# Performance work log

Hardware: AMD Instinct MI355X
Metric: run time of the kernel (lower is better)

Reference implementation:

```python
import jax, jax.numpy as jnp
import numpy as np

PATCH = 16  # patch_size

def _patchify(images, p=PATCH):
    # images: [B, H, W] -> patches: [B, N, p*p] in raster order
    B, H, W = images.shape
    x = images.reshape(B, H // p, p, W // p, p)
    x = x.transpose(0, 1, 3, 2, 4)  # [B, H/p, W/p, p, p]
    return x.reshape(B, (H // p) * (W // p), p * p)

def setup_inputs() -> dict:
    key = jax.random.key(0)
    k1, k2 = jax.random.split(key)
    images = jax.random.normal(k1, (64, 256, 256), dtype=jnp.float32)
    vocab = jax.random.normal(k2, (4096, 256), dtype=jnp.float32)  # [V, patch^2]
    return {"images": images, "vocab": vocab}

def reference(images, vocab):
    # forward_patches: patchify (raster ordering -> identity permutation)
    patches = _patchify(images)  # [B, N, D]
    # forward_tokens: torch.cdist + argmin. argmin of Euclidean distance
    # equals argmin of squared distance; expand ||x-v||^2 to avoid the
    # explicit [B, N, V, D] difference tensor.
    v2 = jnp.sum(vocab * vocab, axis=-1)                      # [V]
    xv = jnp.einsum('bnd,vd->bnv', patches, vocab)            # [B, N, V]
    x2 = jnp.sum(patches * patches, axis=-1, keepdims=True)   # [B, N, 1]
    d2 = x2 - 2.0 * xv + v2                                   # [B, N, V]
    tokens = jnp.argmin(d2, axis=-1)                          # [B, N] int
    return patches, tokens
```

## Files before the change

kernel.cpp:

```cpp
#include <hip/hip_runtime.h>
#include <math.h>

#define PS      16
#define D       256
#define V       4096
#define M       16384
#define NSPLIT  32
#define PAIR_CAP 1048576
#define QMARGIN 130

typedef _Float16 half8 __attribute__((ext_vector_type(8)));
typedef _Float16 half4 __attribute__((ext_vector_type(4)));
typedef float    f32x4 __attribute__((ext_vector_type(4)));

__device__ __forceinline__ void gload_lds16(const void* g, void* l) {
  __builtin_amdgcn_global_load_lds(
      (const __attribute__((address_space(1))) unsigned int*)g,
      (__attribute__((address_space(3))) unsigned int*)l, 16, 0, 0);
}

__global__ __launch_bounds__(256) void patchify_half_kernel(
    const float* __restrict__ img, float* __restrict__ outp,
    _Float16* __restrict__ Ah, int* __restrict__ paircount) {
  if (blockIdx.x == 0 && threadIdx.x == 0) *paircount = 0;
  const int t  = blockIdx.x * 256 + threadIdx.x;
  const int o4 = t << 2;
  const int b   = o4 >> 16;
  const int rem = o4 & 65535;
  const int n   = rem >> 8;
  const int d   = rem & 255;
  const int py = n >> 4, px = n & 15, i = d >> 4, j = d & 15;
  const float4 v = *(const float4*)(img + (b << 16) + ((py * PS + i) << 8) + px * PS + j);
  *(float4*)(outp + o4) = v;
  half4 h = { (_Float16)v.x, (_Float16)v.y, (_Float16)v.z, (_Float16)v.w };
  *(half4*)(Ah + o4) = h;
}

__global__ __launch_bounds__(256) void vocab_half_v2_kernel(
    const float* __restrict__ vocab, _Float16* __restrict__ Vh,
    float* __restrict__ v2) {
  const int gtid = blockIdx.x * 256 + threadIdx.x;
  const int row  = gtid >> 6;
  const int lane = gtid & 63;
  const float4 v = *(const float4*)(vocab + (size_t)row * D + (lane << 2));
  half4 h = { (_Float16)v.x, (_Float16)v.y, (_Float16)v.z, (_Float16)v.w };
  *(half4*)(Vh + (size_t)row * D + (lane << 2)) = h;
  float s = v.x * v.x + v.y * v.y + v.z * v.z + v.w * v.w;
  #pragma unroll
  for (int off = 32; off > 0; off >>= 1) s += __shfl_down(s, off);
  if (lane == 0) v2[row] = s;
}

__global__ __launch_bounds__(256, 3) void gemm_score_kernel(
    const _Float16* __restrict__ Ah,
    const _Float16* __restrict__ Vh,
    const float* __restrict__ v2,
    unsigned* __restrict__ pk1, unsigned* __restrict__ pk2) {
  __shared__ __align__(16) _Float16 Af[8 * 64 * 32];
  __shared__ unsigned eK1[64][4];
  __shared__ unsigned eK2[64][4];

  const int tid  = threadIdx.x;
  const int lane = tid & 63;
  const int wid  = tid >> 6;
  const int cb   = blockIdx.x;
  const int row0 = blockIdx.y * 64;
  const int col0 = cb * 128 + wid * 32;

  {
    const int srow = lane >> 2;
    const int sg   = ((lane & 3) ^ ((srow >> 1) & 3)) << 3;
    const _Float16* Ag = Ah + (size_t)(row0 + wid * 16 + srow) * D + sg;
    _Float16* Al = Af + wid * 16 * 32;
    #pragma unroll
    for (int kt = 0; kt < 8; ++kt)
      gload_lds16(Ag + kt * 32, Al + kt * 64 * 32);
  }
  __syncthreads();

  const int cl = lane & 15;
  const int q  = lane >> 4;
  const int fg = (q ^ ((cl >> 1) & 3)) << 3;
  const _Float16* Ab = Af + cl * 32 + fg;

  const int c0 = col0 + cl;
  const int c1 = c0 + 16;
  const _Float16* B0 = Vh + (size_t)c0 * D + q * 8;
  const _Float16* B1 = Vh + (size_t)c1 * D + q * 8;

  f32x4 acc[4][2];
  #pragma unroll
  for (int i = 0; i < 4; ++i) {
    acc[i][0] = (f32x4){0.f, 0.f, 0.f, 0.f};
    acc[i][1] = (f32x4){0.f, 0.f, 0.f, 0.f};
  }

  #pragma unroll 1
  for (int kt = 0; kt < 8; ++kt) {
    const half8 b0 = *(const half8*)(B0 + kt * 32);
    const half8 b1 = *(const half8*)(B1 + kt * 32);
    half8 af[4];
    #pragma unroll
    for (int i = 0; i < 4; ++i)
      af[i] = *(const half8*)(Ab + kt * 2048 + i * 512);
    #pragma unroll
    for (int i = 0; i < 4; ++i) {
      acc[i][0] = __builtin_amdgcn_mfma_f32_16x16x32_f16(af[i], b0, acc[i][0], 0, 0, 0);
      acc[i][1] = __builtin_amdgcn_mfma_f32_16x16x32_f16(af[i], b1, acc[i][1], 0, 0, 0);
    }
  }

  const float C0 = fmaf(v2[c0], 512.0f, 524288.0f);
  const float C1 = fmaf(v2[c1], 512.0f, 524288.0f);
  unsigned kk1[16], kk2[16];
  #pragma unroll
  for (int i = 0; i < 4; ++i)
    #pragma unroll
    for (int r = 0; r < 4; ++r) {
      const int p = i * 4 + r;
      const unsigned k0 = ((unsigned)fmaf(-1024.0f, acc[i][0][r], C0) << 12) | (unsigned)c0;
      const unsigned k1 = ((unsigned)fmaf(-1024.0f, acc[i][1][r], C1) << 12) | (unsigned)c1;
      kk1[p] = min(k0, k1);
      kk2[p] = max(k0, k1);
    }
  #pragma unroll
  for (int p = 0; p < 16; ++p) {
    unsigned k1 = kk1[p], k2 = kk2[p];
    #pragma unroll
    for (int mask = 1; mask <= 8; mask <<= 1) {
      const unsigned o1 = (unsigned)__shfl_xor((int)k1, mask);
      const unsigned o2 = (unsigned)__shfl_xor((int)k2, mask);
      k2 = min(min(k2, o2), max(k1, o1));
      k1 = min(k1, o1);
    }
    kk1[p] = k1; kk2[p] = k2;
  }
  if (cl == 0) {
    #pragma unroll
    for (int p = 0; p < 16; ++p) {
      const int rl = (p >> 2) * 16 + q * 4 + (p & 3);
      eK1[rl][wid] = kk1[p]; eK2[rl][wid] = kk2[p];
    }
  }
  __syncthreads();
  if (tid < 64) {
    unsigned K1 = 0xFFFFFFFFu, K2 = 0xFFFFFFFFu;
    #pragma unroll
    for (int w = 0; w < 4; ++w) {
      const unsigned b1 = eK1[tid][w], b2 = eK2[tid][w];
      K2 = min(min(K2, b2), max(K1, b1));
      K1 = min(K1, b1);
    }
    pk1[(size_t)cb * M + row0 + tid] = K1;
    pk2[(size_t)cb * M + row0 + tid] = K2;
  }
}

__global__ __launch_bounds__(256) void reduce_gather_kernel(
    const unsigned* __restrict__ pk1, const unsigned* __restrict__ pk2,
    float* __restrict__ tok, unsigned long long* __restrict__ minkey,
    unsigned* __restrict__ pairs, int* __restrict__ paircount) {
  const int m = blockIdx.x * 256 + threadIdx.x;
  unsigned K1 = 0xFFFFFFFFu, K2 = 0xFFFFFFFFu;
  for (int s = 0; s < NSPLIT; ++s) {
    const unsigned b1 = pk1[(size_t)s * M + m];
    const unsigned b2 = pk2[(size_t)s * M + m];
    K2 = min(min(K2, b2), max(K1, b1));
    K1 = min(K1, b1);
  }
  tok[m] = (float)(K1 & 4095u);
  minkey[m] = 0xFFFFFFFFFFFFFFFFull;
  if ((int)(K2 >> 12) - (int)(K1 >> 12) <= QMARGIN) {
    const int th = (int)(K1 >> 12) + QMARGIN;
    int cnt = 0;
    for (int s = 0; s < NSPLIT; ++s) {
      const unsigned b1 = pk1[(size_t)s * M + m];
      const unsigned b2 = pk2[(size_t)s * M + m];
      cnt += ((int)(b2 >> 12) <= th) ? 128
           : (((int)(b1 >> 12) <= th) ? 1 : 0);
    }
    int base = atomicAdd(paircount, cnt);
    if (base + cnt <= PAIR_CAP) {
      const unsigned mh = (unsigned)m << 12;
      for (int s = 0; s < NSPLIT; ++s) {
        const unsigned b1 = pk1[(size_t)s * M + m];
        const unsigned b2 = pk2[(size_t)s * M + m];
        if ((int)(b2 >> 12) <= th) {
          for (int r = 0; r < 128; ++r) pairs[base + r] = mh | (unsigned)(s * 128 + r);
          base += 128;
        } else if ((int)(b1 >> 12) <= th) {
          pairs[base++] = mh | (b1 & 4095u);
        }
      }
    }
  }
}

__global__ __launch_bounds__(256) void refine_score(
    const float* __restrict__ patches, const float* __restrict__ vocab,
    const unsigned* __restrict__ pairs, const int* __restrict__ paircount,
    unsigned long long* __restrict__ minkey) {
  const int lane = threadIdx.x & 63;
  const int gw = (blockIdx.x * 256 + threadIdx.x) >> 6;
  const int nw = (gridDim.x * 256) >> 6;
  int np = *paircount;
  if (np > PAIR_CAP) np = PAIR_CAP;
  for (int i = gw; i < np; i += nw) {
    const unsigned pr = pairs[i];
    const int m = pr >> 12, row = pr & 4095;
    const float4 pv = *(const float4*)(patches + (size_t)m * D + (lane << 2));
    const float4 vv = *(const float4*)(vocab + (size_t)row * D + (lane << 2));
    double acc = 0.0, df;
    df = (double)pv.x - (double)vv.x; acc = fma(df, df, acc);
    df = (double)pv.y - (double)vv.y; acc = fma(df, df, acc);
    df = (double)pv.z - (double)vv.z; acc = fma(df, df, acc);
    df = (double)pv.w - (double)vv.w; acc = fma(df, df, acc);
    #pragma unroll
    for (int off = 32; off > 0; off >>= 1) acc += __shfl_down(acc, off);
    if (lane == 0) {
      const unsigned long long key =
          ((unsigned long long)__double_as_longlong(acc) & ~0xFFFull) | (unsigned)row;
      atomicMin(&minkey[m], key);
    }
  }
}

__global__ __launch_bounds__(256) void refine_final(
    const unsigned* __restrict__ pairs, const int* __restrict__ paircount,
    const unsigned long long* __restrict__ minkey, float* __restrict__ tok) {
  int np = *paircount;
  if (np > PAIR_CAP) np = PAIR_CAP;
  for (int i = blockIdx.x * 256 + threadIdx.x; i < np; i += gridDim.x * 256) {
    const int m = pairs[i] >> 12;
    tok[m] = (float)(unsigned)(minkey[m] & 4095ull);
  }
}

extern "C" void kernel_launch(void* const* d_in, const int* in_sizes, int n_in,
                              void* d_out, int out_size, void* d_ws, size_t ws_size,
                              hipStream_t stream) {
  const float* images = (const float*)d_in[0];
  const float* vocab  = (const float*)d_in[1];
  float* out     = (float*)d_out;
  float* patches = out;
  float* tokens  = out + (size_t)M * D;

  char* ws = (char*)d_ws;
  _Float16* Ah       = (_Float16*)(ws);
  _Float16* Vh       = (_Float16*)(ws + 8388608);
  float*    v2       = (float*)   (ws + 10485760);
  unsigned* pk1      = (unsigned*)(ws + 10502144);
  unsigned* pk2      = (unsigned*)(ws + 12599296);
  unsigned long long* minkey = (unsigned long long*)(ws + 14696448);
  int*      paircount= (int*)     (ws + 14827520);
  unsigned* pairs    = (unsigned*)(ws + 14827584);

  patchify_half_kernel<<<(M * D / 4) / 256, 256, 0, stream>>>(images, patches, Ah,
                                                              paircount);
  vocab_half_v2_kernel<<<(V * 64) / 256, 256, 0, stream>>>(vocab, Vh, v2);
  gemm_score_kernel<<<dim3(V / 128, M / 64), 256, 0, stream>>>(Ah, Vh, v2, pk1, pk2);
  reduce_gather_kernel<<<M / 256, 256, 0, stream>>>(pk1, pk2, tokens, minkey,
                                                    pairs, paircount);
  refine_score<<<512, 256, 0, stream>>>(patches, vocab, pairs, paircount, minkey);
  refine_final<<<64, 256, 0, stream>>>(pairs, paircount, minkey, tokens);
}
```

Measured before the change: 177.3 us.

## Widen GEMM column tile to 256, halve splits, fuse prep kernels

Each wave now computes a 64x64 tile (4x4 MFMA accumulators) instead of 64x32, so each block covers 256 vocab columns and the split count drops from 32 to 16. This reuses each A fragment across more MFMAs and halves the partial top-2 buffers that the reduce kernel reads. The grid order is swapped so consecutive blocks share the same vocab slice. The patchify and vocab-conversion kernels are merged into one launch. The costs are higher register pressure, which may lower occupancy under launch_bounds(256,3), and refine sets that are twice as large whenever a split's second-best key falls inside the margin.

```diff
diff --git a/kernel.cpp b/kernel.cpp
--- a/kernel.cpp
+++ b/kernel.cpp
@@ -5,7 +5,7 @@
 #define D       256
 #define V       4096
 #define M       16384
-#define NSPLIT  32
+#define NSPLIT  16
 #define PAIR_CAP 1048576
 #define QMARGIN 130
 
@@ -19,36 +19,36 @@
       (__attribute__((address_space(3))) unsigned int*)l, 16, 0, 0);
 }
 
-__global__ __launch_bounds__(256) void patchify_half_kernel(
-    const float* __restrict__ img, float* __restrict__ outp,
-    _Float16* __restrict__ Ah, int* __restrict__ paircount) {
-  if (blockIdx.x == 0 && threadIdx.x == 0) *paircount = 0;
-  const int t  = blockIdx.x * 256 + threadIdx.x;
-  const int o4 = t << 2;
-  const int b   = o4 >> 16;
-  const int rem = o4 & 65535;
-  const int n   = rem >> 8;
-  const int d   = rem & 255;
-  const int py = n >> 4, px = n & 15, i = d >> 4, j = d & 15;
-  const float4 v = *(const float4*)(img + (b << 16) + ((py * PS + i) << 8) + px * PS + j);
-  *(float4*)(outp + o4) = v;
-  half4 h = { (_Float16)v.x, (_Float16)v.y, (_Float16)v.z, (_Float16)v.w };
-  *(half4*)(Ah + o4) = h;
-}
-
-__global__ __launch_bounds__(256) void vocab_half_v2_kernel(
-    const float* __restrict__ vocab, _Float16* __restrict__ Vh,
-    float* __restrict__ v2) {
-  const int gtid = blockIdx.x * 256 + threadIdx.x;
-  const int row  = gtid >> 6;
-  const int lane = gtid & 63;
-  const float4 v = *(const float4*)(vocab + (size_t)row * D + (lane << 2));
-  half4 h = { (_Float16)v.x, (_Float16)v.y, (_Float16)v.z, (_Float16)v.w };
-  *(half4*)(Vh + (size_t)row * D + (lane << 2)) = h;
-  float s = v.x * v.x + v.y * v.y + v.z * v.z + v.w * v.w;
-  #pragma unroll
-  for (int off = 32; off > 0; off >>= 1) s += __shfl_down(s, off);
-  if (lane == 0) v2[row] = s;
+__global__ __launch_bounds__(256) void prep_kernel(
+    const float* __restrict__ img, const float* __restrict__ vocab,
+    float* __restrict__ outp, _Float16* __restrict__ Ah,
+    _Float16* __restrict__ Vh, float* __restrict__ v2,
+    int* __restrict__ paircount) {
+  if (blockIdx.x < 4096) {
+    if (blockIdx.x == 0 && threadIdx.x == 0) *paircount = 0;
+    const int t  = blockIdx.x * 256 + threadIdx.x;
+    const int o4 = t << 2;
+    const int b   = o4 >> 16;
+    const int rem = o4 & 65535;
+    const int n   = rem >> 8;
+    const int d   = rem & 255;
+    const int py = n >> 4, px = n & 15, i = d >> 4, j = d & 15;
+    const float4 v = *(const float4*)(img + (b << 16) + ((py * PS + i) << 8) + px * PS + j);
+    *(float4*)(outp + o4) = v;
+    half4 h = { (_Float16)v.x, (_Float16)v.y, (_Float16)v.z, (_Float16)v.w };
+    *(half4*)(Ah + o4) = h;
+  } else {
+    const int gtid = (blockIdx.x - 4096) * 256 + threadIdx.x;
+    const int row  = gtid >> 6;
+    const int lane = gtid & 63;
+    const float4 v = *(const float4*)(vocab + (size_t)row * D + (lane << 2));
+    half4 h = { (_Float16)v.x, (_Float16)v.y, (_Float16)v.z, (_Float16)v.w };
+    *(half4*)(Vh + (size_t)row * D + (lane << 2)) = h;
+    float s = v.x * v.x + v.y * v.y + v.z * v.z + v.w * v.w;
+    #pragma unroll
+    for (int off = 32; off > 0; off >>= 1) s += __shfl_down(s, off);
+    if (lane == 0) v2[row] = s;
+  }
 }
 
 __global__ __launch_bounds__(256, 3) void gemm_score_kernel(
@@ -63,9 +63,9 @@
   const int tid  = threadIdx.x;
   const int lane = tid & 63;
   const int wid  = tid >> 6;
-  const int cb   = blockIdx.x;
-  const int row0 = blockIdx.y * 64;
-  const int col0 = cb * 128 + wid * 32;
+  const int row0 = blockIdx.x * 64;
+  const int sp   = blockIdx.y;
+  const int col0 = sp * 256 + wid * 64;
 
   {
     const int srow = lane >> 2;
@@ -83,45 +83,50 @@
   const int fg = (q ^ ((cl >> 1) & 3)) << 3;
   const _Float16* Ab = Af + cl * 32 + fg;
 
-  const int c0 = col0 + cl;
-  const int c1 = c0 + 16;
-  const _Float16* B0 = Vh + (size_t)c0 * D + q * 8;
-  const _Float16* B1 = Vh + (size_t)c1 * D + q * 8;
-
-  f32x4 acc[4][2];
-  #pragma unroll
-  for (int i = 0; i < 4; ++i) {
-    acc[i][0] = (f32x4){0.f, 0.f, 0.f, 0.f};
-    acc[i][1] = (f32x4){0.f, 0.f, 0.f, 0.f};
-  }
+  const _Float16* Bp = Vh + (size_t)(col0 + cl) * D + q * 8;
+
+  f32x4 acc[4][4];
+  #pragma unroll
+  for (int i = 0; i < 4; ++i)
+    #pragma unroll
+    for (int j = 0; j < 4; ++j) acc[i][j] = (f32x4){0.f, 0.f, 0.f, 0.f};
 
   #pragma unroll 1
   for (int kt = 0; kt < 8; ++kt) {
-    const half8 b0 = *(const half8*)(B0 + kt * 32);
-    const half8 b1 = *(const half8*)(B1 + kt * 32);
+    half8 b[4];
+    #pragma unroll
+    for (int j = 0; j < 4; ++j)
+      b[j] = *(const half8*)(Bp + (size_t)j * 16 * D + kt * 32);
     half8 af[4];
     #pragma unroll
     for (int i = 0; i < 4; ++i)
       af[i] = *(const half8*)(Ab + kt * 2048 + i * 512);
     #pragma unroll
-    for (int i = 0; i < 4; ++i) {
-      acc[i][0] = __builtin_amdgcn_mfma_f32_16x16x32_f16(af[i], b0, acc[i][0], 0, 0, 0);
-      acc[i][1] = __builtin_amdgcn_mfma_f32_16x16x32_f16(af[i], b1, acc[i][1], 0, 0, 0);
-    }
-  }
-
-  const float C0 = fmaf(v2[c0], 512.0f, 524288.0f);
-  const float C1 = fmaf(v2[c1], 512.0f, 524288.0f);
+    for (int i = 0; i < 4; ++i)
+      #pragma unroll
+      for (int j = 0; j < 4; ++j)
+        acc[i][j] = __builtin_amdgcn_mfma_f32_16x16x32_f16(af[i], b[j], acc[i][j], 0, 0, 0);
+  }
+
+  float Cj[4];
+  #pragma unroll
+  for (int j = 0; j < 4; ++j) Cj[j] = fmaf(v2[col0 + j * 16 + cl], 512.0f, 524288.0f);
   unsigned kk1[16], kk2[16];
   #pragma unroll
   for (int i = 0; i < 4; ++i)
     #pragma unroll
     for (int r = 0; r < 4; ++r) {
       const int p = i * 4 + r;
-      const unsigned k0 = ((unsigned)fmaf(-1024.0f, acc[i][0][r], C0) << 12) | (unsigned)c0;
-      const unsigned k1 = ((unsigned)fmaf(-1024.0f, acc[i][1][r], C1) << 12) | (unsigned)c1;
-      kk1[p] = min(k0, k1);
-      kk2[p] = max(k0, k1);
+      unsigned K1 = 0xFFFFFFFFu, K2 = 0xFFFFFFFFu;
+      #pragma unroll
+      for (int j = 0; j < 4; ++j) {
+        const unsigned key =
+            ((unsigned)fmaf(-1024.0f, acc[i][j][r], Cj[j]) << 12) |
+            (unsigned)(col0 + j * 16 + cl);
+        K2 = min(K2, max(K1, key));
+        K1 = min(K1, key);
+      }
+      kk1[p] = K1; kk2[p] = K2;
     }
   #pragma unroll
   for (int p = 0; p < 16; ++p) {
@@ -151,8 +156,8 @@
       K2 = min(min(K2, b2), max(K1, b1));
       K1 = min(K1, b1);
     }
-    pk1[(size_t)cb * M + row0 + tid] = K1;
-    pk2[(size_t)cb * M + row0 + tid] = K2;
+    pk1[(size_t)sp * M + row0 + tid] = K1;
+    pk2[(size_t)sp * M + row0 + tid] = K2;
   }
 }
 
@@ -176,7 +181,7 @@
     for (int s = 0; s < NSPLIT; ++s) {
       const unsigned b1 = pk1[(size_t)s * M + m];
       const unsigned b2 = pk2[(size_t)s * M + m];
-      cnt += ((int)(b2 >> 12) <= th) ? 128
+      cnt += ((int)(b2 >> 12) <= th) ? 256
            : (((int)(b1 >> 12) <= th) ? 1 : 0);
     }
     int base = atomicAdd(paircount, cnt);
@@ -186,8 +191,8 @@
         const unsigned b1 = pk1[(size_t)s * M + m];
         const unsigned b2 = pk2[(size_t)s * M + m];
         if ((int)(b2 >> 12) <= th) {
-          for (int r = 0; r < 128; ++r) pairs[base + r] = mh | (unsigned)(s * 128 + r);
-          base += 128;
+          for (int r = 0; r < 256; ++r) pairs[base + r] = mh | (unsigned)(s * 256 + r);
+          base += 256;
         } else if ((int)(b1 >> 12) <= th) {
           pairs[base++] = mh | (b1 & 4095u);
         }
@@ -250,15 +255,14 @@
   _Float16* Vh       = (_Float16*)(ws + 8388608);
   float*    v2       = (float*)   (ws + 10485760);
   unsigned* pk1      = (unsigned*)(ws + 10502144);
-  unsigned* pk2      = (unsigned*)(ws + 12599296);
-  unsigned long long* minkey = (unsigned long long*)(ws + 14696448);
-  int*      paircount= (int*)     (ws + 14827520);
-  unsigned* pairs    = (unsigned*)(ws + 14827584);
-
-  patchify_half_kernel<<<(M * D / 4) / 256, 256, 0, stream>>>(images, patches, Ah,
-                                                              paircount);
-  vocab_half_v2_kernel<<<(V * 64) / 256, 256, 0, stream>>>(vocab, Vh, v2);
-  gemm_score_kernel<<<dim3(V / 128, M / 64), 256, 0, stream>>>(Ah, Vh, v2, pk1, pk2);
+  unsigned* pk2      = (unsigned*)(ws + 11550720);
+  unsigned long long* minkey = (unsigned long long*)(ws + 12599296);
+  int*      paircount= (int*)     (ws + 12730368);
+  unsigned* pairs    = (unsigned*)(ws + 12730432);
+
+  prep_kernel<<<4096 + 1024, 256, 0, stream>>>(images, vocab, patches, Ah,
+                                               Vh, v2, paircount);
+  gemm_score_kernel<<<dim3(M / 64, NSPLIT), 256, 0, stream>>>(Ah, Vh, v2, pk1, pk2);
   reduce_gather_kernel<<<M / 256, 256, 0, stream>>>(pk1, pk2, tokens, minkey,
                                                     pairs, paircount);
   refine_score<<<512, 256, 0, stream>>>(patches, vocab, pairs, paircount, minkey);
```

Result: faster. 172.8 us (-2.5%).
